# Optimization experiments

Measured on AMD Instinct MI355X. Metric: run time of the kernel, lower is better.

The kernel has to match this reference:

```python
import jax, jax.numpy as jnp
import numpy as np

B, N, D = 64, 197, 768
H, HD = 12, 64
MAX_REL = 14
SCALE = HD ** -0.5


def rel_indices(n, max_rel):
    """Static 2D relative-position index matrices of shape (n, n), int32."""
    lq = n - 1
    side = int(lq ** 0.5)
    r = np.arange(lq)
    dv = r[None, :] // side - r[:, None] // side
    dh = r[None, :] % side - r[:, None] % side
    fv = np.clip(dv, -max_rel, max_rel) + max_rel + 1
    fh = np.clip(dh, -max_rel, max_rel) + max_rel + 1
    # pad one row/col of zeros on top-left for the cls token (index 0)
    fv = np.pad(fv, ((1, 0), (1, 0)), constant_values=0)
    fh = np.pad(fh, ((1, 0), (1, 0)), constant_values=0)
    return fv.astype(np.int32), fh.astype(np.int32)


IDX_V, IDX_H = rel_indices(N, MAX_REL)


def setup_inputs() -> dict:
    key = jax.random.key(0)
    ks = jax.random.split(key, 13)
    lin = lambda k: jax.random.normal(k, (D, H * HD), jnp.float32) * 0.02
    tab = lambda k: jax.random.normal(k, (2 * MAX_REL + 2, HD), jnp.float32) * 0.02
    return {
        'x': jax.random.normal(ks[0], (B, N, D), jnp.float32),
        'wq': lin(ks[1]), 'bq': jnp.zeros((H * HD,), jnp.float32),
        'wk': lin(ks[2]), 'bk': jnp.zeros((H * HD,), jnp.float32),
        'wv': lin(ks[3]), 'bv': jnp.zeros((H * HD,), jnp.float32),
        'wp': jax.random.normal(ks[4], (H * HD, D), jnp.float32) * 0.02,
        'bp': jnp.zeros((D,), jnp.float32),
        'rel_k_v': tab(ks[5]), 'rel_k_h': tab(ks[6]),
        'rel_v_v': tab(ks[7]), 'rel_v_h': tab(ks[8]),
    }


def reference(x, wq, bq, wk, bk, wv, bv, wp, bp, rel_k_v, rel_k_h, rel_v_v, rel_v_h):
    b, n, _ = x.shape
    # qkv projections -> (B, H, N, HD)
    q = (x @ wq + bq).reshape(b, n, H, HD).transpose(0, 2, 1, 3)
    k = (x @ wk + bk).reshape(b, n, H, HD).transpose(0, 2, 1, 3)
    v = (x @ wv + bv).reshape(b, n, H, HD).transpose(0, 2, 1, 3)

    attn = jnp.einsum('bhid,bhjd->bhij', q, k) * SCALE
    # iRPE key bias: gather (N, N, HD) table then contract with q per query pos
    r_p_k = rel_k_v[IDX_V] + rel_k_h[IDX_H]              # (N, N, HD)
    attn = attn + jnp.einsum('bhid,ijd->bhij', q, r_p_k) * SCALE
    attn = jax.nn.softmax(attn, axis=-1)

    out = jnp.einsum('bhij,bhjd->bhid', attn, v)
    # iRPE value bias
    r_p_v = rel_v_v[IDX_V] + rel_v_h[IDX_H]              # (N, N, HD)
    out = out + jnp.einsum('bhij,ijd->bhid', attn, r_p_v)

    out = out.transpose(0, 2, 1, 3).reshape(b, n, H * HD)
    return out @ wp + bp
```

## Files before the change

### kernel.cpp

```cpp
#include <hip/hip_runtime.h>
#include <math.h>

#define SCALE_ 0.125f

typedef unsigned short u16;
typedef __attribute__((ext_vector_type(8))) _Float16 half8;
typedef __attribute__((ext_vector_type(4))) float f32x4;
#define MFMA_H __builtin_amdgcn_mfma_f32_16x16x32_f16

__device__ __forceinline__ u16 f2h(float f) {
    union { _Float16 h; u16 u; } v; v.h = (_Float16)f; return v.u;
}
__device__ __forceinline__ float h2f(u16 u) {
    union { _Float16 h; u16 u; } v; v.u = u; return (float)v.h;
}
__device__ __forceinline__ void gload16(const u16* g, u16* l) {
    __builtin_amdgcn_global_load_lds(
        (const __attribute__((address_space(1))) void*)g,
        (__attribute__((address_space(3))) void*)l, 16, 0, 0);
}
__device__ __forceinline__ half8 ld_h8(const u16* p) {
    return *(const half8*)p;
}

__global__ void prep_all(const float* __restrict__ x,
                         const float* __restrict__ w0, const float* __restrict__ w1,
                         const float* __restrict__ w2, const float* __restrict__ w3,
                         const float* __restrict__ rkv, const float* __restrict__ rkh,
                         const float* __restrict__ rvv, const float* __restrict__ rvh,
                         u16* __restrict__ xh,
                         u16* o0, u16* o1, u16* o2, u16* o3,
                         u16* __restrict__ tk, u16* __restrict__ gt,
                         u16* __restrict__ khot, u16* __restrict__ vtp) {
    __shared__ float t[64 * 68];
    int b = blockIdx.x;
    const int tid = threadIdx.x;

    if (b < 4728) {
        size_t idx = ((size_t)b * 256 + tid) * 8;
        float4 a = *(const float4*)(x + idx), bb = *(const float4*)(x + idx + 4);
        float f[8] = {a.x, a.y, a.z, a.w, bb.x, bb.y, bb.z, bb.w};
        u16 hs[8];
        #pragma unroll
        for (int e = 0; e < 8; ++e) hs[e] = f2h(f[e]);
        *(uint4*)(xh + idx) = *(uint4*)hs;
        return;
    }
    b -= 4728;
    if (b < 576) {
        int z = b / 144, rem = b - z * 144;
        int by = rem / 12, bx = rem - by * 12;
        const float* W; u16* oh;
        if (z == 0)      { W = w0; oh = o0; }
        else if (z == 1) { W = w1; oh = o1; }
        else if (z == 2) { W = w2; oh = o2; }
        else             { W = w3; oh = o3; }
        int k0 = by * 64, n0 = bx * 64;
        #pragma unroll
        for (int rr = 0; rr < 4; ++rr) {
            int r = (tid >> 4) + rr * 16;
            int c = (tid & 15) * 4;
            *(float4*)&t[r * 68 + c] = *(const float4*)(W + (size_t)(k0 + r) * 768 + n0 + c);
        }
        __syncthreads();
        int n = tid >> 2, kc = (tid & 3) * 16;
        u16 hs[16];
        #pragma unroll
        for (int e = 0; e < 16; ++e) hs[e] = f2h(t[(kc + e) * 68 + n]);
        size_t o = (size_t)(n0 + n) * 768 + k0 + kc;
        *(uint4*)(oh + o) = *(uint4*)hs;
        *(uint4*)(oh + o + 8) = *(uint4*)(hs + 8);
        return;
    }
    b -= 576;
    if (b < 16) {
        int idx = b * 256 + tid;
        int r = idx >> 6, d = idx & 63;
        float tv = 0.f;
        if (r < 30) tv = rkv[r * 64 + d];
        else if (r >= 32 && r < 62) tv = rkh[(r - 32) * 64 + d];
        tk[idx] = f2h(tv);
        return;
    }
    b -= 16;
    if (b < 28) {
        int idx = b * 256 + tid;
        int g = idx / 224, j = idx - (idx / 224) * 224;
        float v = 0.f;
        if (j >= 1 && j < 197) {
            int jq = j - 1;
            int jv = jq / 14, jh = jq - jv * 14;
            if (g < 14) v = (jv == g) ? 1.f : 0.f;
            else if (g >= 16 && g < 30) v = (jh == g - 16) ? 1.f : 0.f;
        }
        gt[idx] = f2h(v);
        return;
    }
    b -= 28;
    if (b < 28) {
        int idx = b * 256 + tid;
        int j = idx >> 5, c = idx & 31;
        float v = 0.f;
        if (j >= 1 && j < 197) {
            int jq = j - 1;
            int jv = jq / 14, jh = jq - jv * 14;
            if (c < 14) v = (jv == c) ? 1.f : 0.f;
            else if (c < 28) v = (jh == c - 14) ? 1.f : 0.f;
        }
        khot[idx] = f2h(v);
        return;
    }
    b -= 28;
    {
        u16* vb = vtp + (size_t)b * 64 * 288;
        for (int tt = tid; tt < 64 * 91; tt += 256) {
            int d = tt / 91;
            int c = 197 + (tt - d * 91);
            u16 val = 0;
            if (c >= 208 && c < 272) {
                int rr = c - 208;
                float v = 0.f;
                if (rr < 30) v = rvv[rr * 64 + d];
                else if (rr >= 32 && rr < 62) v = rvh[(rr - 32) * 64 + d];
                val = f2h(v);
            }
            vb[d * 288 + c] = val;
        }
    }
}

__global__ __launch_bounds__(256, 4) void gemm_f16(
    const u16* __restrict__ Ah,
    const u16* __restrict__ B0, const u16* __restrict__ B1, const u16* __restrict__ B2,
    const float* __restrict__ bias0, const float* __restrict__ bias1,
    const float* __restrict__ bias2,
    u16* qo, u16* ko, u16* vo, float* outf, int nz, int kind)
{
    __shared__ u16 SM[128 * 134 + 1024];
    u16* As = SM;
    u16* Bs = SM + 128 * 64;

    const int p = blockIdx.x;
    const int xcd = p & 7, s = p >> 3;
    const int mcnt = (xcd < 3) ? 13 : 12;
    const int mbase = (xcd < 3) ? xcd * 13 : 39 + (xcd - 3) * 12;
    const int jn = 6 * nz;
    if (s >= mcnt * jn) return;
    const int mb = mbase + s / jn;
    const int j = s % jn;
    const int z = j / 6;
    const int nb = j % 6;

    const u16* Bt = B0; const float* bias = bias0;
    if (z == 1) { Bt = B1; bias = bias1; }
    else if (z == 2) { Bt = B2; bias = bias2; }

    const int m0 = mb * 128, n0 = nb * 128;
    const int tid = threadIdx.x;
    const int w = tid >> 6, lane = tid & 63, quad = lane >> 4, l16 = lane & 15;
    const int wm = (w >> 1) * 64, wn = (w & 1) * 64;
    const int rl8 = lane >> 3, cs = lane & 7;
    const int csrc = (cs ^ rl8) * 8;

    f32x4 acc[4][4];
    #pragma unroll
    for (int a = 0; a < 4; ++a)
        #pragma unroll
        for (int b = 0; b < 4; ++b) acc[a][b] = (f32x4){0, 0, 0, 0};

    for (int kt = 0; kt < 768; kt += 64) {
        __syncthreads();
        #pragma unroll
        for (int i = 0; i < 4; ++i) {
            int r = w * 32 + i * 8 + rl8;
            int arow = min(m0 + r, 12607);
            gload16(Ah + (size_t)arow * 768 + kt + csrc, &As[(w * 32 + i * 8) * 64]);
            gload16(Bt + (size_t)(n0 + r) * 768 + kt + csrc, &Bs[(w * 32 + i * 8) * 64]);
        }
        __syncthreads();
        #pragma unroll
        for (int kb = 0; kb < 2; ++kb) {
            const int slot = ((kb * 4 + quad) ^ (l16 & 7)) * 8;
            half8 ah[4], bf[4];
            #pragma unroll
            for (int mi = 0; mi < 4; ++mi) {
                ah[mi] = ld_h8(&As[(wm + mi * 16 + l16) * 64 + slot]);
                bf[mi] = ld_h8(&Bs[(wn + mi * 16 + l16) * 64 + slot]);
            }
            #pragma unroll
            for (int ni = 0; ni < 4; ++ni)
                #pragma unroll
                for (int mi = 0; mi < 4; ++mi)
                    acc[mi][ni] = MFMA_H(ah[mi], bf[ni], acc[mi][ni], 0, 0, 0);
        }
    }

    if (kind == 1) {
        #pragma unroll
        for (int mi = 0; mi < 4; ++mi) {
            #pragma unroll
            for (int r = 0; r < 4; ++r) {
                int gr = m0 + wm + mi * 16 + quad * 4 + r;
                if (gr >= 12608) continue;
                #pragma unroll
                for (int ni = 0; ni < 4; ++ni) {
                    int gc = n0 + wn + ni * 16 + l16;
                    outf[(size_t)gr * 768 + gc] = acc[mi][ni][r] + bias[gc];
                }
            }
        }
        return;
    }

    __syncthreads();

    if (z == 2) {
        u16* Ct = SM;
        #pragma unroll
        for (int mi = 0; mi < 4; ++mi) {
            #pragma unroll
            for (int ni = 0; ni < 4; ++ni) {
                int col = wn + ni * 16 + l16;
                float bv = bias[n0 + col];
                #pragma unroll
                for (int r = 0; r < 4; ++r)
                    Ct[col * 134 + (wm + mi * 16 + quad * 4 + r)] =
                        f2h(acc[mi][ni][r] + bv);
            }
        }
        __syncthreads();
        int k2 = tid & 127, chalf = tid >> 7;
        int gr = m0 + k2;
        if (gr < 12608) {
            int bb = gr / 197, ii = gr - bb * 197;
            int h = (n0 >> 6) + chalf;
            u16* vbase = vo + ((size_t)(bb * 12 + h) * 64) * 288 + ii;
            #pragma unroll
            for (int dd = 0; dd < 64; ++dd)
                vbase[(size_t)dd * 288] = Ct[(chalf * 64 + dd) * 134 + k2];
        }
        return;
    }

    u16* Cs = SM;
    #pragma unroll
    for (int mi = 0; mi < 4; ++mi) {
        #pragma unroll
        for (int ni = 0; ni < 4; ++ni) {
            int col = wn + ni * 16 + l16;
            float bv = bias[n0 + col];
            #pragma unroll
            for (int r = 0; r < 4; ++r)
                Cs[(wm + mi * 16 + quad * 4 + r) * 128 + col] = f2h(acc[mi][ni][r] + bv);
        }
    }
    __syncthreads();
    u16* O = (z == 0) ? qo : ko;
    int row = tid >> 1, halfc = tid & 1;
    int gr = m0 + row;
    if (gr < 12608) {
        int bb = gr / 197, ii = gr - bb * 197;
        int h = (n0 >> 6) + halfc;
        u16* dst = O + ((size_t)(bb * 12 + h) * 197 + ii) * 64;
        const u16* src = &Cs[row * 128 + halfc * 64];
        #pragma unroll
        for (int e = 0; e < 8; ++e)
            *(uint4*)(dst + e * 8) = *(const uint4*)(src + e * 8);
    }
}

__global__ __launch_bounds__(512, 3) void attn_mfma(
    const u16* __restrict__ qh, const u16* __restrict__ kh,
    const u16* __restrict__ tk, const u16* __restrict__ vt,
    const u16* __restrict__ gt, const u16* __restrict__ khot,
    u16* __restrict__ oh)
{
    __shared__ u16 Ph[64 * 296];
    __shared__ float BsT[64 * 36];
    __shared__ float red[64 * 4];
    u16* Tvh16 = (u16*)BsT;
    u16* Kst = Ph;

    const int p = blockIdx.x;
    const int xcd = p & 7, s = p >> 3;
    const int bh = xcd * 96 + (s >> 2);
    const int qt = s & 3;
    const int I0 = qt * 64;
    const int tid = threadIdx.x;
    const int w = tid >> 6, lane = tid & 63, quad = lane >> 4, l16 = lane & 15;
    const int mf = w >> 1, nh = w & 1;
    const int mr0 = mf * 16;
    const size_t base = (size_t)bh * 197 * 64;
    const uint4 z4 = make_uint4(0, 0, 0, 0);

    half8 qa[2];
    {
        int i = I0 + mr0 + l16;
        bool ok = i < 197;
        const u16* qp = qh + base + (size_t)i * 64 + quad * 8;
        #pragma unroll
        for (int kb = 0; kb < 2; ++kb) {
            uint4 a = ok ? *(const uint4*)(qp + kb * 32) : z4;
            *(uint4*)&qa[kb] = a;
        }
    }
    int jj[7];
    #pragma unroll
    for (int s1 = 0; s1 < 7; ++s1) jj[s1] = (nh * 7 + s1) * 16 + l16;
    half8 kfh[7];
    #pragma unroll
    for (int s1 = 0; s1 < 7; ++s1)
        kfh[s1] = ld_h8(khot + jj[s1] * 32 + quad * 8);
    uint4 kreg[4];
    #pragma unroll
    for (int t2 = 0; t2 < 4; ++t2) {
        int t = tid + t2 * 512;
        int row = t >> 3, chunk = t & 7;
        kreg[t2] = (t < 1792 && row < 197)
                 ? *(const uint4*)(kh + base + (size_t)row * 64 + chunk * 8) : z4;
    }

    #pragma unroll
    for (int s2 = 0; s2 < 2; ++s2) {
        int c = (nh * 2 + s2) * 16 + l16;
        f32x4 acc = (f32x4){0, 0, 0, 0};
        #pragma unroll
        for (int kb = 0; kb < 2; ++kb) {
            half8 th = ld_h8(tk + c * 64 + kb * 32 + quad * 8);
            acc = MFMA_H(qa[kb], th, acc, 0, 0, 0);
        }
        #pragma unroll
        for (int r = 0; r < 4; ++r)
            Tvh16[(mr0 + quad * 4 + r) * 68 + c] = f2h(acc[r]);
    }

    #pragma unroll
    for (int t2 = 0; t2 < 4; ++t2) {
        int t = tid + t2 * 512;
        if (t < 1792) {
            int row = t >> 3, chunk = t & 7;
            *(uint4*)&Kst[row * 72 + chunk * 8] = kreg[t2];
        }
    }
    __syncthreads();

    half8 qa2;
    {
        int m = mr0 + l16;
        int i = I0 + m;
        u16 vals[8];
        if (i >= 1 && i < 197) {
            int qi = i - 1;
            int iv = qi / 14, ih = qi - iv * 14;
            #pragma unroll
            for (int e = 0; e < 8; ++e) {
                int c = quad * 8 + e;
                u16 v = 0;
                if (c < 14)      v = Tvh16[m * 68 + (c - iv + 15)];
                else if (c < 28) v = Tvh16[m * 68 + 32 + ((c - 14) - ih + 15)];
                vals[e] = v;
            }
        } else {
            #pragma unroll
            for (int e = 0; e < 8; ++e) vals[e] = 0;
        }
        *(uint4*)&qa2 = *(uint4*)vals;
    }

    f32x4 sacc[7];
    #pragma unroll
    for (int s1 = 0; s1 < 7; ++s1) {
        int j = jj[s1];
        f32x4 c = MFMA_H(qa[0], ld_h8(&Kst[j * 72 + quad * 8]),
                         (f32x4){0, 0, 0, 0}, 0, 0, 0);
        c = MFMA_H(qa[1], ld_h8(&Kst[j * 72 + 32 + quad * 8]), c, 0, 0, 0);
        c = MFMA_H(qa2, kfh[s1], c, 0, 0, 0);
        sacc[s1] = c;
    }

    #pragma unroll
    for (int r = 0; r < 4; ++r) {
        float mx = sacc[0][r];
        #pragma unroll
        for (int s1 = 1; s1 < 7; ++s1) mx = fmaxf(mx, sacc[s1][r]);
        mx *= SCALE_;
        #pragma unroll
        for (int off = 1; off < 16; off <<= 1) mx = fmaxf(mx, __shfl_xor(mx, off, 64));
        if (l16 == 0) red[(mr0 + quad * 4 + r) * 4 + nh] = mx;
    }
    __syncthreads();

    #pragma unroll
    for (int r = 0; r < 4; ++r) {
        int m = mr0 + quad * 4 + r;
        float M = fmaxf(red[m * 4], red[m * 4 + 1]);
        float sum = 0.f;
        #pragma unroll
        for (int s1 = 0; s1 < 7; ++s1) {
            float pv = (jj[s1] < 197) ? __expf(sacc[s1][r] * SCALE_ - M) : 0.f;
            sacc[s1][r] = pv;
            sum += pv;
        }
        #pragma unroll
        for (int off = 1; off < 16; off <<= 1) sum += __shfl_xor(sum, off, 64);
        if (l16 == 0) red[m * 4 + 2 + nh] = sum;
    }
    #pragma unroll
    for (int s1 = 0; s1 < 7; ++s1) {
        int j = jj[s1];
        if (j < 208) {
            #pragma unroll
            for (int r = 0; r < 4; ++r)
                Ph[(mr0 + quad * 4 + r) * 296 + j] = f2h(sacc[s1][r]);
        }
    }
    #pragma unroll
    for (int t = 0; t < 2; ++t) {
        int ii2 = tid + t * 512;
        Ph[(ii2 >> 4) * 296 + 208 + (ii2 & 15)] = 0;
    }
    __syncthreads();

    {
        f32x4 bacc = (f32x4){0, 0, 0, 0};
        #pragma unroll
        for (int ks = 0; ks < 7; ++ks) {
            half8 ap = ld_h8(&Ph[(mr0 + l16) * 296 + ks * 32 + quad * 8]);
            half8 gp = ld_h8(gt + (nh * 16 + l16) * 224 + ks * 32 + quad * 8);
            bacc = MFMA_H(ap, gp, bacc, 0, 0, 0);
        }
        #pragma unroll
        for (int r = 0; r < 4; ++r)
            BsT[(mr0 + quad * 4 + r) * 36 + nh * 16 + l16] = bacc[r];
    }
    for (int t = tid; t < 64 * 16; t += 512)
        Ph[(t >> 4) * 296 + 272 + (t & 15)] = 0;
    __syncthreads();

    #pragma unroll
    for (int t = 0; t < 8; ++t) {
        int idx = tid + t * 512;
        int m = idx >> 6, c = idx & 63;
        int i = I0 + m;
        float val;
        if (i == 0) {
            val = (c == 0 || c == 32) ? (red[m * 4 + 2] + red[m * 4 + 3]) : 0.f;
        } else {
            int qi = i - 1;
            int iv = qi / 14, ih = qi - (qi / 14) * 14;
            int r = c & 31;
            int bidx = r + ((c < 32) ? iv : ih) - 15;
            bool ok = (bidx >= 0) && (bidx <= 13) && (r < 30);
            int src = ((c < 32) ? 0 : 16) + min(13, max(0, bidx));
            val = ok ? BsT[m * 36 + src] : 0.f;
            if (r == 0) val += h2f(Ph[m * 296]);
        }
        Ph[m * 296 + 208 + c] = f2h(val);
    }
    __syncthreads();

    {
        f32x4 oacc[2] = {(f32x4){0, 0, 0, 0}, (f32x4){0, 0, 0, 0}};
        const u16* vb = vt + (size_t)bh * 64 * 288;
        #pragma unroll
        for (int ks = 0; ks < 9; ++ks) {
            half8 ap = ld_h8(&Ph[(mr0 + l16) * 296 + ks * 32 + quad * 8]);
            #pragma unroll
            for (int sd = 0; sd < 2; ++sd) {
                int d = (nh * 2 + sd) * 16 + l16;
                half8 bv = ld_h8(vb + (size_t)d * 288 + ks * 32 + quad * 8);
                oacc[sd] = MFMA_H(ap, bv, oacc[sd], 0, 0, 0);
            }
        }
        int b = bh / 12, h = bh - b * 12;
        float rl[4];
        #pragma unroll
        for (int r = 0; r < 4; ++r) {
            int m = mr0 + quad * 4 + r;
            rl[r] = 1.f / (red[m * 4 + 2] + red[m * 4 + 3]);
        }
        #pragma unroll
        for (int sd = 0; sd < 2; ++sd) {
            int d = (nh * 2 + sd) * 16 + l16;
            #pragma unroll
            for (int r = 0; r < 4; ++r) {
                int i = I0 + mr0 + quad * 4 + r;
                if (i < 197) {
                    oh[((size_t)(b * 197 + i)) * 768 + h * 64 + d] =
                        f2h(oacc[sd][r] * rl[r]);
                }
            }
        }
    }
}

extern "C" void kernel_launch(void* const* d_in, const int* in_sizes, int n_in,
                              void* d_out, int out_size, void* d_ws, size_t ws_size,
                              hipStream_t stream)
{
    const float* x   = (const float*)d_in[0];
    const float* wq  = (const float*)d_in[1];
    const float* bq  = (const float*)d_in[2];
    const float* wk  = (const float*)d_in[3];
    const float* bk  = (const float*)d_in[4];
    const float* wv  = (const float*)d_in[5];
    const float* bv  = (const float*)d_in[6];
    const float* wp  = (const float*)d_in[7];
    const float* bp  = (const float*)d_in[8];
    const float* rkv = (const float*)d_in[9];
    const float* rkh = (const float*)d_in[10];
    const float* rvv = (const float*)d_in[11];
    const float* rvh = (const float*)d_in[12];
    float* out = (float*)d_out;

    const size_t SZX = (size_t)12608 * 768;
    const size_t SZW = (size_t)768 * 768;
    const size_t SZVT = (size_t)768 * 64 * 288;

    u16* xh  = (u16*)d_ws;
    u16* qh_ = xh + SZX;
    u16* kh_ = qh_ + SZX;
    u16* vt  = kh_ + SZX;
    u16* wt  = vt + SZVT;
    u16* wqh = wt;
    u16* wkh = wt + SZW;
    u16* wvh = wt + 2 * SZW;
    u16* wph = wt + 3 * SZW;
    u16* tk  = wt + 4 * SZW;
    u16* gt  = tk + 4096;
    u16* khot = gt + 32 * 224;
    u16* oh_ = xh;

    prep_all<<<6144, 256, 0, stream>>>(
        x, wq, wk, wv, wp, rkv, rkh, rvv, rvh,
        xh, wqh, wkh, wvh, wph, tk, gt, khot, vt);

    gemm_f16<<<1872, 256, 0, stream>>>(
        xh, wqh, wkh, wvh, bq, bk, bv, qh_, kh_, vt, nullptr, 3, 0);

    attn_mfma<<<3072, 512, 0, stream>>>(qh_, kh_, tk, vt, gt, khot, oh_);

    gemm_f16<<<624, 256, 0, stream>>>(
        oh_, wph, wph, wph, bp, bp, bp, nullptr, nullptr, nullptr, out, 1, 1);
}
```

Baseline: 285.4 us.

## Double-buffer GEMM LDS tiles with K-step of 32 and a single barrier

Reworks the f16 GEMM main loop into a two-stage pipeline. The next K-slice of A and B is issued via global_load_lds into the alternate buffer while MFMAs consume the current one. The K tile drops from 64 to 32, and each 64-element LDS line now packs two rows with an XOR swizzle, so the double buffer fits in the same shared allocation. The aim is to overlap global-to-LDS transfer with compute and cut from two barriers per K-step to one. The cost is twice as many loop iterations with fewer MFMAs per barrier.

```diff
diff --git a/kernel.cpp b/kernel.cpp
--- a/kernel.cpp
+++ b/kernel.cpp
@@ -136,9 +136,7 @@
     const float* __restrict__ bias2,
     u16* qo, u16* ko, u16* vo, float* outf, int nz, int kind)
 {
-    __shared__ u16 SM[128 * 134 + 1024];
-    u16* As = SM;
-    u16* Bs = SM + 128 * 64;
+    __shared__ u16 SM[18176];
 
     const int p = blockIdx.x;
     const int xcd = p & 7, s = p >> 3;
@@ -159,8 +157,17 @@
     const int tid = threadIdx.x;
     const int w = tid >> 6, lane = tid & 63, quad = lane >> 4, l16 = lane & 15;
     const int wm = (w >> 1) * 64, wn = (w & 1) * 64;
-    const int rl8 = lane >> 3, cs = lane & 7;
-    const int csrc = (cs ^ rl8) * 8;
+
+    const int t0 = w * 64 + lane;
+    const int t1 = (4 + w) * 64 + lane;
+    const int sr0 = t0 >> 3, c80 = (t0 & 7) ^ (sr0 & 7);
+    const int sr1 = t1 >> 3, c81 = (t1 & 7) ^ (sr1 & 7);
+    const int ar0 = sr0 * 2 + (c80 >> 2), ac0 = (c80 & 3) * 8;
+    const int ar1 = sr1 * 2 + (c81 >> 2), ac1 = (c81 & 3) * 8;
+    const u16* Asrc0 = Ah + (size_t)min(m0 + ar0, 12607) * 768 + ac0;
+    const u16* Asrc1 = Ah + (size_t)min(m0 + ar1, 12607) * 768 + ac1;
+    const u16* Bsrc0 = Bt + (size_t)(n0 + ar0) * 768 + ac0;
+    const u16* Bsrc1 = Bt + (size_t)(n0 + ar1) * 768 + ac1;
 
     f32x4 acc[4][4];
     #pragma unroll
@@ -168,31 +175,40 @@
         #pragma unroll
         for (int b = 0; b < 4; ++b) acc[a][b] = (f32x4){0, 0, 0, 0};
 
-    for (int kt = 0; kt < 768; kt += 64) {
+    auto STAGE = [&](int buf, int kt) {
+        u16* Ab = SM + buf * 8192;
+        u16* Bb = Ab + 4096;
+        gload16(Asrc0 + kt, Ab + w * 512);
+        gload16(Asrc1 + kt, Ab + (4 + w) * 512);
+        gload16(Bsrc0 + kt, Bb + w * 512);
+        gload16(Bsrc1 + kt, Bb + (4 + w) * 512);
+    };
+    auto COMPUTE = [&](int buf) {
+        u16* Ab = SM + buf * 8192;
+        u16* Bb = Ab + 4096;
+        half8 ah[4], bf[4];
+        #pragma unroll
+        for (int mi = 0; mi < 4; ++mi) {
+            int R = wm + mi * 16 + l16;
+            ah[mi] = ld_h8(Ab + (R >> 1) * 64 +
+                           ((((R & 1) * 4 + quad) ^ ((R >> 1) & 7)) * 8));
+            int Rn = wn + mi * 16 + l16;
+            bf[mi] = ld_h8(Bb + (Rn >> 1) * 64 +
+                           ((((Rn & 1) * 4 + quad) ^ ((Rn >> 1) & 7)) * 8));
+        }
+        #pragma unroll
+        for (int ni = 0; ni < 4; ++ni)
+            #pragma unroll
+            for (int mi = 0; mi < 4; ++mi)
+                acc[mi][ni] = MFMA_H(ah[mi], bf[ni], acc[mi][ni], 0, 0, 0);
+    };
+
+    STAGE(0, 0);
+    __syncthreads();
+    for (int it = 0; it < 24; ++it) {
+        if (it < 23) STAGE((it + 1) & 1, (it + 1) * 32);
+        COMPUTE(it & 1);
         __syncthreads();
-        #pragma unroll
-        for (int i = 0; i < 4; ++i) {
-            int r = w * 32 + i * 8 + rl8;
-            int arow = min(m0 + r, 12607);
-            gload16(Ah + (size_t)arow * 768 + kt + csrc, &As[(w * 32 + i * 8) * 64]);
-            gload16(Bt + (size_t)(n0 + r) * 768 + kt + csrc, &Bs[(w * 32 + i * 8) * 64]);
-        }
-        __syncthreads();
-        #pragma unroll
-        for (int kb = 0; kb < 2; ++kb) {
-            const int slot = ((kb * 4 + quad) ^ (l16 & 7)) * 8;
-            half8 ah[4], bf[4];
-            #pragma unroll
-            for (int mi = 0; mi < 4; ++mi) {
-                ah[mi] = ld_h8(&As[(wm + mi * 16 + l16) * 64 + slot]);
-                bf[mi] = ld_h8(&Bs[(wn + mi * 16 + l16) * 64 + slot]);
-            }
-            #pragma unroll
-            for (int ni = 0; ni < 4; ++ni)
-                #pragma unroll
-                for (int mi = 0; mi < 4; ++mi)
-                    acc[mi][ni] = MFMA_H(ah[mi], bf[ni], acc[mi][ni], 0, 0, 0);
-        }
     }
 
     if (kind == 1) {
@@ -211,8 +227,6 @@
         }
         return;
     }
-
-    __syncthreads();
 
     if (z == 2) {
         u16* Ct = SM;
```

Result: slower. 299.8 us (+5.0%).
